# Optimization experiments

Measured on AMD Instinct MI355X. Metric: run time of the kernel, lower is better.

The kernel has to match this reference:

```python
import jax, jax.numpy as jnp
import numpy as np

N = 50000      # nodes
E = 800000     # edges (avg degree 16)
D = 64         # num_node_features
H = 64         # hidden_channels
G = 512        # graphs in batch
OUT = 32       # final linear output
NEG_SLOPE = 0.2


def setup_inputs() -> dict:
    key = jax.random.key(0)
    ks = jax.random.split(key, 20)
    s = 0.1  # param init scale
    inp = {
        "x": jax.random.normal(ks[0], (N, D), jnp.float32),
        "edge_index": jax.random.randint(ks[1], (2, E), 0, N, dtype=jnp.int64),
        "batch": jnp.sort(jax.random.randint(ks[2], (N,), 0, G, dtype=jnp.int64)),
        # GATv2 layer 1 (D -> H)
        "Wl1": jax.random.normal(ks[3], (D, H), jnp.float32) * s,
        "bl1": jnp.zeros((H,), jnp.float32),
        "Wr1": jax.random.normal(ks[4], (D, H), jnp.float32) * s,
        "br1": jnp.zeros((H,), jnp.float32),
        "att1": jax.random.normal(ks[5], (H,), jnp.float32) * s,
        "bias1": jnp.zeros((H,), jnp.float32),
        # GATv2 layer 2 (H -> H)
        "Wl2": jax.random.normal(ks[6], (H, H), jnp.float32) * s,
        "bl2": jnp.zeros((H,), jnp.float32),
        "Wr2": jax.random.normal(ks[7], (H, H), jnp.float32) * s,
        "br2": jnp.zeros((H,), jnp.float32),
        "att2": jax.random.normal(ks[8], (H,), jnp.float32) * s,
        "bias2": jnp.zeros((H,), jnp.float32),
        # final classifier
        "lin_w": jax.random.normal(ks[9], (H, OUT), jnp.float32) * s,
        "lin_b": jnp.zeros((OUT,), jnp.float32),
    }
    return inp


def _gatv2(x, src, dst, Wl, bl, Wr, br, att, bias):
    # GATv2Conv, heads=1, PyG semantics: messages flow src -> dst
    xl = x @ Wl + bl                       # [N, H] source transform (also the message)
    xr = x @ Wr + br                       # [N, H] destination transform
    z = xl[src] + xr[dst]                  # [E, H] gather
    e = jax.nn.leaky_relu(z, NEG_SLOPE) @ att  # [E] edge scores
    # segment softmax over edges grouped by destination node
    m = jax.ops.segment_max(e, dst, num_segments=N)   # [N]
    ex = jnp.exp(e - m[dst])                          # [E]
    denom = jax.ops.segment_sum(ex, dst, num_segments=N)  # [N]
    alpha = ex / denom[dst]                            # [E]
    out = jax.ops.segment_sum(alpha[:, None] * xl[src], dst, num_segments=N)  # [N, H]
    return out + bias


def reference(x, edge_index, batch,
              Wl1, bl1, Wr1, br1, att1, bias1,
              Wl2, bl2, Wr2, br2, att2, bias2,
              lin_w, lin_b):
    src, dst = edge_index[0], edge_index[1]
    h = jax.nn.relu(_gatv2(x, src, dst, Wl1, bl1, Wr1, br1, att1, bias1))
    h = jax.nn.relu(_gatv2(h, src, dst, Wl2, bl2, Wr2, br2, att2, bias2))
    # global mean pool over graphs
    sums = jax.ops.segment_sum(h, batch, num_segments=G)          # [G, H]
    cnts = jax.ops.segment_sum(jnp.ones((h.shape[0],), h.dtype), batch, num_segments=G)
    pooled = sums / jnp.maximum(cnts, 1.0)[:, None]
    # dropout(p=0.5) is identity at inference
    return pooled @ lin_w + lin_b                                  # [G, 32]
```

## Files before the change

kernel.cpp:

```cpp
#include <hip/hip_runtime.h>
#include <hip/hip_fp16.h>
#include <math.h>


#define ELLC    48
#define OVF_CAP 65536
#define ECHUNK  2048

typedef int      vint4 __attribute__((ext_vector_type(4)));
typedef _Float16 half4 __attribute__((ext_vector_type(4)));
typedef float    f32x4 __attribute__((ext_vector_type(4)));

#define GROWS 32
template <typename T>
__device__ __forceinline__ void dual_gemm_slim(
    int bid, int t,
    const T* __restrict__ X,
    const float* __restrict__ Wl, const float* __restrict__ bl,
    const float* __restrict__ Wr, const float* __restrict__ br,
    _Float16* __restrict__ xl, float* __restrict__ xr, int n,
    float* xS) {
    int row0 = bid * GROWS;
    for (int i = t; i < GROWS * 16; i += 256) {
        int r = row0 + (i >> 4);
        f32x4 v;
        v[0] = 0.f; v[1] = 0.f; v[2] = 0.f; v[3] = 0.f;
        if (r < n) {
            if constexpr (sizeof(T) == 2) {
                half4 hv = __builtin_nontemporal_load(
                    &((const half4*)(X + (size_t)r * 64))[i & 15]);
                v[0] = (float)hv[0]; v[1] = (float)hv[1];
                v[2] = (float)hv[2]; v[3] = (float)hv[3];
            } else {
                v = __builtin_nontemporal_load(
                    &((const f32x4*)(X + (size_t)r * 64))[i & 15]);
            }
        }
        ((f32x4*)xS)[i] = v;
    }
    __syncthreads();
    int h  = t & 63;
    int rb = t >> 6;
    float accl[8], accr[8];
#pragma unroll
    for (int i = 0; i < 8; ++i) { accl[i] = 0.f; accr[i] = 0.f; }
#pragma unroll 4
    for (int d = 0; d < 64; ++d) {
        float wl = Wl[d * 64 + h];
        float wr = Wr[d * 64 + h];
#pragma unroll
        for (int i = 0; i < 8; ++i) {
            float xv = xS[(rb + 4 * i) * 64 + d];
            accl[i] += xv * wl;
            accr[i] += xv * wr;
        }
    }
    float blv = bl[h], brv = br[h];
#pragma unroll
    for (int i = 0; i < 8; ++i) {
        int r = row0 + rb + 4 * i;
        if (r < n) {
            __builtin_nontemporal_store((_Float16)(accl[i] + blv),
                                        &xl[(size_t)r * 64 + h]);
            __builtin_nontemporal_store(accr[i] + brv,
                                        &xr[(size_t)r * 64 + h]);
        }
    }
}

__global__ __launch_bounds__(256) void dual_gemm64_f16_kernel(
    const _Float16* __restrict__ X,
    const float* __restrict__ Wl, const float* __restrict__ bl,
    const float* __restrict__ Wr, const float* __restrict__ br,
    _Float16* __restrict__ xl, float* __restrict__ xr, int n) {
    __shared__ float xS[GROWS * 64];
    dual_gemm_slim<_Float16>(blockIdx.x, threadIdx.x, X, Wl, bl, Wr, br,
                             xl, xr, n, xS);
}

__global__ __launch_bounds__(256) void fill_gemm_kernel(
    const int* __restrict__ src, const int* __restrict__ dst,
    int* __restrict__ cnt, unsigned short* __restrict__ ell,
    int* __restrict__ novf, int* __restrict__ ovf_dst, int* __restrict__ ovf_src,
    int E, int N, int psize, int fb, int ggrid,
    const float* __restrict__ X,
    const float* __restrict__ Wl, const float* __restrict__ bl,
    const float* __restrict__ Wr, const float* __restrict__ br,
    _Float16* __restrict__ xl, float* __restrict__ xr) {
    __shared__ float xS[GROWS * 64];
    int b = blockIdx.x;
    int q = b / 24, r = b % 24;
    if (r >= 16) {
        int vg = q * 8 + (r - 16);
        if (vg < ggrid)
            dual_gemm_slim<float>(vg, threadIdx.x, X, Wl, bl, Wr, br,
                                  xl, xr, N, xS);
        return;
    }
    int vb = q * 16 + r;
    if (vb >= fb) return;
    int t     = threadIdx.x;
    int chunk = vb >> 3;
    int p     = vb & 7;
    int d0    = p * psize;
    int d1    = min(N, d0 + psize);
    int e0    = chunk * ECHUNK;
    int e1    = min(E, e0 + ECHUNK);
    int nq    = (e1 - e0) >> 2;
    const vint4* dst4 = (const vint4*)(dst + e0);
    const vint4* src4 = (const vint4*)(src + e0);

    auto scatter4 = [&](vint4 dv, vint4 sv) {
#pragma unroll
        for (int k = 0; k < 4; ++k) {
            int d = dv[k];
            int s = sv[k];
            if (d >= d0 && d < d1) {
                int pos = atomicAdd(&cnt[d], 1);
                if (pos < ELLC) {
                    ell[d * ELLC + pos] = (unsigned short)s;
                } else {
                    int j = atomicAdd(novf, 1);
                    if (j < OVF_CAP) { ovf_dst[j] = d; ovf_src[j] = s; }
                }
            }
        }
    };

    if (nq == (ECHUNK >> 2)) {
        vint4 dvA = __builtin_nontemporal_load(&dst4[t]);
        vint4 svA = __builtin_nontemporal_load(&src4[t]);
        vint4 dvB = __builtin_nontemporal_load(&dst4[t + 256]);
        vint4 svB = __builtin_nontemporal_load(&src4[t + 256]);
        scatter4(dvA, svA);
        scatter4(dvB, svB);
    } else {
        for (int qq = t; qq < nq; qq += 256) {
            vint4 dv = __builtin_nontemporal_load(&dst4[qq]);
            vint4 sv = __builtin_nontemporal_load(&src4[qq]);
            scatter4(dv, sv);
        }
        for (int e = e0 + (nq << 2) + t; e < e1; e += 256) {
            int d = dst[e];
            if (d >= d0 && d < d1) {
                int pos = atomicAdd(&cnt[d], 1);
                int s   = src[e];
                if (pos < ELLC) {
                    ell[d * ELLC + pos] = (unsigned short)s;
                } else {
                    int j = atomicAdd(novf, 1);
                    if (j < OVF_CAP) { ovf_dst[j] = d; ovf_src[j] = s; }
                }
            }
        }
    }
}

__global__ __launch_bounds__(256) void gat_aggregate_kernel(
    const _Float16* __restrict__ xl, const float* __restrict__ xr,
    const int* __restrict__ cnt, const unsigned short* __restrict__ ell,
    const int* __restrict__ novf, const int* __restrict__ ovf_dst,
    const int* __restrict__ ovf_src,
    const float* __restrict__ att, const float* __restrict__ bias,
    _Float16* __restrict__ out, int n) {
    int wid  = (blockIdx.x * blockDim.x + threadIdx.x) >> 6;
    int lane = threadIdx.x & 63;
    if (wid >= n) return;
    int g = lane >> 4;
    int l = lane & 15;
    int d = wid;

    float4 att4 = ((const float4*)att)[l];
    float4 b4   = ((const float4*)bias)[l];
    int deg_d = cnt[d];
    int nd  = min(deg_d, ELLC);
    int beg = d * ELLC;

    float  s   = 0.f;
    float4 acc = make_float4(0.f, 0.f, 0.f, 0.f);

    if (deg_d > 0) {
        int myidx = 0;
        if (lane < ELLC)
            myidx = (int)__builtin_nontemporal_load(&ell[beg + lane]);
        int i_first = __shfl(myidx, 0);

        f32x4 xrt = __builtin_nontemporal_load(
            &((const f32x4*)(xr + (size_t)d * 64))[l]);
        float4 xr4 = make_float4(xrt[0], xrt[1], xrt[2], xrt[3]);

#pragma unroll 6
        for (int k = 0; k * 8 < nd; ++k) {
            int  sa = k * 8 + g, sb = sa + 4;
            bool aa = sa < nd,   ab = sb < nd;
            int  i0 = __shfl(myidx, sa); if (!aa) i0 = i_first;
            int  i1 = __shfl(myidx, sb); if (!ab) i1 = i_first;
            half4 h0 = ((const half4*)(xl + (size_t)i0 * 64))[l];
            half4 h1 = ((const half4*)(xl + (size_t)i1 * 64))[l];
            float4 x0 = make_float4((float)h0[0], (float)h0[1], (float)h0[2], (float)h0[3]);
            float4 x1 = make_float4((float)h1[0], (float)h1[1], (float)h1[2], (float)h1[3]);
            float z, c0 = 0.f, c1 = 0.f;
            z = x0.x + xr4.x; c0 += ((z > 0.f) ? z : 0.2f * z) * att4.x;
            z = x0.y + xr4.y; c0 += ((z > 0.f) ? z : 0.2f * z) * att4.y;
            z = x0.z + xr4.z; c0 += ((z > 0.f) ? z : 0.2f * z) * att4.z;
            z = x0.w + xr4.w; c0 += ((z > 0.f) ? z : 0.2f * z) * att4.w;
            z = x1.x + xr4.x; c1 += ((z > 0.f) ? z : 0.2f * z) * att4.x;
            z = x1.y + xr4.y; c1 += ((z > 0.f) ? z : 0.2f * z) * att4.y;
            z = x1.z + xr4.z; c1 += ((z > 0.f) ? z : 0.2f * z) * att4.z;
            z = x1.w + xr4.w; c1 += ((z > 0.f) ? z : 0.2f * z) * att4.w;
#pragma unroll
            for (int sh = 8; sh >= 1; sh >>= 1) {
                c0 += __shfl_xor(c0, sh);
                c1 += __shfl_xor(c1, sh);
            }
            float w0 = aa ? __expf(fminf(c0, 30.f)) : 0.f;
            float w1 = ab ? __expf(fminf(c1, 30.f)) : 0.f;
            s += w0 + w1;
            acc.x += w0 * x0.x + w1 * x1.x;
            acc.y += w0 * x0.y + w1 * x1.y;
            acc.z += w0 * x0.z + w1 * x1.z;
            acc.w += w0 * x0.w + w1 * x1.w;
        }
        if (deg_d > ELLC) {
            int no = min(*novf, OVF_CAP);
            for (int j = g; j < no; j += 4) {
                bool active = (ovf_dst[j] == d);
                int  i0     = active ? ovf_src[j] : i_first;
                half4 h0 = ((const half4*)(xl + (size_t)i0 * 64))[l];
                float4 x0 = make_float4((float)h0[0], (float)h0[1], (float)h0[2], (float)h0[3]);
                float z, c0 = 0.f;
                z = x0.x + xr4.x; c0 += ((z > 0.f) ? z : 0.2f * z) * att4.x;
                z = x0.y + xr4.y; c0 += ((z > 0.f) ? z : 0.2f * z) * att4.y;
                z = x0.z + xr4.z; c0 += ((z > 0.f) ? z : 0.2f * z) * att4.z;
                z = x0.w + xr4.w; c0 += ((z > 0.f) ? z : 0.2f * z) * att4.w;
#pragma unroll
                for (int sh = 8; sh >= 1; sh >>= 1) c0 += __shfl_xor(c0, sh);
                float w0 = active ? __expf(fminf(c0, 30.f)) : 0.f;
                s += w0;
                acc.x += w0 * x0.x;
                acc.y += w0 * x0.y;
                acc.z += w0 * x0.z;
                acc.w += w0 * x0.w;
            }
        }
#pragma unroll
        for (int mask = 16; mask <= 32; mask <<= 1) {
            s     += __shfl_xor(s, mask);
            acc.x += __shfl_xor(acc.x, mask);
            acc.y += __shfl_xor(acc.y, mask);
            acc.z += __shfl_xor(acc.z, mask);
            acc.w += __shfl_xor(acc.w, mask);
        }
    }
    if (g == 0) {
        float inv = (s > 0.f) ? (1.f / s) : 0.f;
        half4 hv;
        hv[0] = (_Float16)fmaxf(acc.x * inv + b4.x, 0.f);
        hv[1] = (_Float16)fmaxf(acc.y * inv + b4.y, 0.f);
        hv[2] = (_Float16)fmaxf(acc.z * inv + b4.z, 0.f);
        hv[3] = (_Float16)fmaxf(acc.w * inv + b4.w, 0.f);
        __builtin_nontemporal_store(hv, (half4*)(out + (size_t)d * 64) + l);
    }
}

__global__ __launch_bounds__(256) void pool_final_kernel(
    const _Float16* __restrict__ h, const int* __restrict__ batch,
    const float* __restrict__ lin_w, const float* __restrict__ lin_b,
    float* __restrict__ out, int N, int G) {
    int g = blockIdx.x;
    int t = threadIdx.x;
    auto lb = [&](int key) {
        int lo = 0, hi = N;
        while (lo < hi) {
            int mid = (lo + hi) >> 1;
            if (batch[mid] < key) lo = mid + 1; else hi = mid;
        }
        return lo;
    };
    int start = lb(g), end = lb(g + 1);

    __shared__ float part[4][64];
    __shared__ float pooled[64];
    int f = t & 63, w = t >> 6;
    float acc = 0.f;
    for (int i = start + w; i < end; i += 4)
        acc += (float)__builtin_nontemporal_load(&h[(size_t)i * 64 + f]);
    part[w][f] = acc;
    __syncthreads();
    if (t < 64) {
        float s = part[0][t] + part[1][t] + part[2][t] + part[3][t];
        pooled[t] = s / fmaxf((float)(end - start), 1.f);
    }
    __syncthreads();
    if (t < 32) {
        float a = 0.f;
#pragma unroll 8
        for (int hh = 0; hh < 64; ++hh) a += pooled[hh] * lin_w[hh * 32 + t];
        out[g * 32 + t] = a + lin_b[t];
    }
}

extern "C" void kernel_launch(void* const* d_in, const int* in_sizes, int n_in,
                              void* d_out, int out_size, void* d_ws, size_t ws_size,
                              hipStream_t stream) {
    const float* x     = (const float*)d_in[0];
    const int*   ei    = (const int*)d_in[1];
    const int*   batch = (const int*)d_in[2];
    const float* Wl1   = (const float*)d_in[3];
    const float* bl1   = (const float*)d_in[4];
    const float* Wr1   = (const float*)d_in[5];
    const float* br1   = (const float*)d_in[6];
    const float* att1  = (const float*)d_in[7];
    const float* bias1 = (const float*)d_in[8];
    const float* Wl2   = (const float*)d_in[9];
    const float* bl2   = (const float*)d_in[10];
    const float* Wr2   = (const float*)d_in[11];
    const float* br2   = (const float*)d_in[12];
    const float* att2  = (const float*)d_in[13];
    const float* bias2 = (const float*)d_in[14];
    const float* lin_w = (const float*)d_in[15];
    const float* lin_b = (const float*)d_in[16];
    float* out = (float*)d_out;

    const int N = in_sizes[0] / 64;
    const int E = in_sizes[1] / 2;
    const int G = out_size / 32;
    const int* src = ei;
    const int* dst = ei + E;

    char*  ws  = (char*)d_ws;
    size_t off = 0;
    auto alloc = [&](size_t bytes) -> void* {
        void* p = ws + off;
        off += bytes;
        off = (off + 255) & ~(size_t)255;
        return p;
    };
    _Float16* xl   = (_Float16*)alloc((size_t)N * 64 * sizeof(_Float16));
    float* xr      = (float*)alloc((size_t)N * 64 * sizeof(float));
    _Float16* h1   = (_Float16*)alloc((size_t)N * 64 * sizeof(_Float16));
    int*   cnt     = (int*)alloc((size_t)N * sizeof(int));
    int*   novf    = (int*)alloc(256);
    char*  zend    = ws + off;
    unsigned short* ell = (unsigned short*)alloc((size_t)N * ELLC * sizeof(unsigned short));
    int*   ovf_dst = (int*)alloc((size_t)OVF_CAP * sizeof(int));
    int*   ovf_src = (int*)alloc((size_t)OVF_CAP * sizeof(int));

    (void)hipMemsetAsync(cnt, 0, (size_t)(zend - (char*)cnt), stream);

    int ggrid  = (N + GROWS - 1) / GROWS;
    int agrid  = (N + 3) / 4;
    int nchunk = (E + ECHUNK - 1) / ECHUNK;
    int fb     = nchunk * 8;
    int psize  = (N + 7) / 8;
    int ngroups = max((fb + 15) / 16, (ggrid + 7) / 8);
    int igrid   = ngroups * 24;

    fill_gemm_kernel<<<igrid, 256, 0, stream>>>(
        src, dst, cnt, ell, novf, ovf_dst, ovf_src, E, N, psize, fb, ggrid,
        x, Wl1, bl1, Wr1, br1, xl, xr);

    gat_aggregate_kernel<<<agrid, 256, 0, stream>>>(
        xl, xr, cnt, ell, novf, ovf_dst, ovf_src, att1, bias1, h1, N);

    dual_gemm64_f16_kernel<<<ggrid, 256, 0, stream>>>(
        h1, Wl2, bl2, Wr2, br2, xl, xr, N);

    gat_aggregate_kernel<<<agrid, 256, 0, stream>>>(
        xl, xr, cnt, ell, novf, ovf_dst, ovf_src, att2, bias2, h1, N);

    pool_final_kernel<<<G, 256, 0, stream>>>(h1, batch, lin_w, lin_b, out, N, G);
}
```

Measured before the change: 249.6 us.

## Fuse layer-1 aggregation with layer-2 dual GEMM via shared-memory staging

Replaces the separate layer-1 aggregate kernel and the layer-2 dual GEMM kernel with one kernel. Each block aggregates 32 destination rows (8 per wavefront) into LDS in fp32, then runs the dual GEMM on them directly. This removes a launch and the fp16 h1 round trip through global memory, and drops the fp16 rounding of h1. In exchange each block processes rows serially per wave, which lowers parallelism for the gather-heavy phase, and separate xl2/xr2 buffers are allocated.

```diff
diff --git a/kernel.cpp b/kernel.cpp
--- a/kernel.cpp
+++ b/kernel.cpp
@@ -12,33 +12,26 @@
 typedef float    f32x4 __attribute__((ext_vector_type(4)));
 
 #define GROWS 32
-template <typename T>
-__device__ __forceinline__ void dual_gemm_slim(
-    int bid, int t,
-    const T* __restrict__ X,
-    const float* __restrict__ Wl, const float* __restrict__ bl,
-    const float* __restrict__ Wr, const float* __restrict__ br,
-    _Float16* __restrict__ xl, float* __restrict__ xr, int n,
-    float* xS) {
-    int row0 = bid * GROWS;
+
+__device__ __forceinline__ void stage_rows_f32(
+    int row0, int t, const float* __restrict__ X, int n, float* xS) {
     for (int i = t; i < GROWS * 16; i += 256) {
         int r = row0 + (i >> 4);
         f32x4 v;
         v[0] = 0.f; v[1] = 0.f; v[2] = 0.f; v[3] = 0.f;
-        if (r < n) {
-            if constexpr (sizeof(T) == 2) {
-                half4 hv = __builtin_nontemporal_load(
-                    &((const half4*)(X + (size_t)r * 64))[i & 15]);
-                v[0] = (float)hv[0]; v[1] = (float)hv[1];
-                v[2] = (float)hv[2]; v[3] = (float)hv[3];
-            } else {
-                v = __builtin_nontemporal_load(
-                    &((const f32x4*)(X + (size_t)r * 64))[i & 15]);
-            }
-        }
+        if (r < n)
+            v = __builtin_nontemporal_load(
+                &((const f32x4*)(X + (size_t)r * 64))[i & 15]);
         ((f32x4*)xS)[i] = v;
     }
-    __syncthreads();
+}
+
+__device__ __forceinline__ void gemm_compute(
+    int row0, int t,
+    const float* __restrict__ Wl, const float* __restrict__ bl,
+    const float* __restrict__ Wr, const float* __restrict__ br,
+    _Float16* __restrict__ xl, float* __restrict__ xr, int n,
+    const float* xS) {
     int h  = t & 63;
     int rb = t >> 6;
     float accl[8], accr[8];
@@ -66,16 +59,6 @@
                                         &xr[(size_t)r * 64 + h]);
         }
     }
-}
-
-__global__ __launch_bounds__(256) void dual_gemm64_f16_kernel(
-    const _Float16* __restrict__ X,
-    const float* __restrict__ Wl, const float* __restrict__ bl,
-    const float* __restrict__ Wr, const float* __restrict__ br,
-    _Float16* __restrict__ xl, float* __restrict__ xr, int n) {
-    __shared__ float xS[GROWS * 64];
-    dual_gemm_slim<_Float16>(blockIdx.x, threadIdx.x, X, Wl, bl, Wr, br,
-                             xl, xr, n, xS);
 }
 
 __global__ __launch_bounds__(256) void fill_gemm_kernel(
@@ -92,9 +75,11 @@
     int q = b / 24, r = b % 24;
     if (r >= 16) {
         int vg = q * 8 + (r - 16);
-        if (vg < ggrid)
-            dual_gemm_slim<float>(vg, threadIdx.x, X, Wl, bl, Wr, br,
-                                  xl, xr, N, xS);
+        if (vg < ggrid) {
+            stage_rows_f32(vg * GROWS, threadIdx.x, X, N, xS);
+            __syncthreads();
+            gemm_compute(vg * GROWS, threadIdx.x, Wl, bl, Wr, br, xl, xr, N, xS);
+        }
         return;
     }
     int vb = q * 16 + r;
@@ -156,6 +141,138 @@
     }
 }
 
+__device__ __forceinline__ void agg_row(
+    int d, int lane, int g, int l,
+    const _Float16* __restrict__ xl, const float* __restrict__ xr,
+    const int* __restrict__ cnt, const unsigned short* __restrict__ ell,
+    const int* __restrict__ novf, const int* __restrict__ ovf_dst,
+    const int* __restrict__ ovf_src,
+    float4 att4, float& s, float4& acc, int& deg_d) {
+    deg_d = cnt[d];
+    int nd  = min(deg_d, ELLC);
+    int beg = d * ELLC;
+    s = 0.f;
+    acc = make_float4(0.f, 0.f, 0.f, 0.f);
+    if (deg_d <= 0) return;
+
+    int myidx = 0;
+    if (lane < ELLC)
+        myidx = (int)__builtin_nontemporal_load(&ell[beg + lane]);
+    int i_first = __shfl(myidx, 0);
+
+    f32x4 xrt = __builtin_nontemporal_load(
+        &((const f32x4*)(xr + (size_t)d * 64))[l]);
+    float4 xr4 = make_float4(xrt[0], xrt[1], xrt[2], xrt[3]);
+
+#pragma unroll 6
+    for (int k = 0; k * 8 < nd; ++k) {
+        int  sa = k * 8 + g, sb = sa + 4;
+        bool aa = sa < nd,   ab = sb < nd;
+        int  i0 = __shfl(myidx, sa); if (!aa) i0 = i_first;
+        int  i1 = __shfl(myidx, sb); if (!ab) i1 = i_first;
+        half4 h0 = ((const half4*)(xl + (size_t)i0 * 64))[l];
+        half4 h1 = ((const half4*)(xl + (size_t)i1 * 64))[l];
+        float4 x0 = make_float4((float)h0[0], (float)h0[1], (float)h0[2], (float)h0[3]);
+        float4 x1 = make_float4((float)h1[0], (float)h1[1], (float)h1[2], (float)h1[3]);
+        float z, c0 = 0.f, c1 = 0.f;
+        z = x0.x + xr4.x; c0 += ((z > 0.f) ? z : 0.2f * z) * att4.x;
+        z = x0.y + xr4.y; c0 += ((z > 0.f) ? z : 0.2f * z) * att4.y;
+        z = x0.z + xr4.z; c0 += ((z > 0.f) ? z : 0.2f * z) * att4.z;
+        z = x0.w + xr4.w; c0 += ((z > 0.f) ? z : 0.2f * z) * att4.w;
+        z = x1.x + xr4.x; c1 += ((z > 0.f) ? z : 0.2f * z) * att4.x;
+        z = x1.y + xr4.y; c1 += ((z > 0.f) ? z : 0.2f * z) * att4.y;
+        z = x1.z + xr4.z; c1 += ((z > 0.f) ? z : 0.2f * z) * att4.z;
+        z = x1.w + xr4.w; c1 += ((z > 0.f) ? z : 0.2f * z) * att4.w;
+#pragma unroll
+        for (int sh = 8; sh >= 1; sh >>= 1) {
+            c0 += __shfl_xor(c0, sh);
+            c1 += __shfl_xor(c1, sh);
+        }
+        float w0 = aa ? __expf(fminf(c0, 30.f)) : 0.f;
+        float w1 = ab ? __expf(fminf(c1, 30.f)) : 0.f;
+        s += w0 + w1;
+        acc.x += w0 * x0.x + w1 * x1.x;
+        acc.y += w0 * x0.y + w1 * x1.y;
+        acc.z += w0 * x0.z + w1 * x1.z;
+        acc.w += w0 * x0.w + w1 * x1.w;
+    }
+    if (deg_d > ELLC) {
+        int no = min(*novf, OVF_CAP);
+        for (int j = g; j < no; j += 4) {
+            bool active = (ovf_dst[j] == d);
+            int  i0     = active ? ovf_src[j] : i_first;
+            half4 h0 = ((const half4*)(xl + (size_t)i0 * 64))[l];
+            float4 x0 = make_float4((float)h0[0], (float)h0[1], (float)h0[2], (float)h0[3]);
+            f32x4 xrt2 = ((const f32x4*)(xr + (size_t)d * 64))[l];
+            float z, c0 = 0.f;
+            z = x0.x + xrt2[0]; c0 += ((z > 0.f) ? z : 0.2f * z) * att4.x;
+            z = x0.y + xrt2[1]; c0 += ((z > 0.f) ? z : 0.2f * z) * att4.y;
+            z = x0.z + xrt2[2]; c0 += ((z > 0.f) ? z : 0.2f * z) * att4.z;
+            z = x0.w + xrt2[3]; c0 += ((z > 0.f) ? z : 0.2f * z) * att4.w;
+#pragma unroll
+            for (int sh = 8; sh >= 1; sh >>= 1) c0 += __shfl_xor(c0, sh);
+            float w0 = active ? __expf(fminf(c0, 30.f)) : 0.f;
+            s += w0;
+            acc.x += w0 * x0.x;
+            acc.y += w0 * x0.y;
+            acc.z += w0 * x0.z;
+            acc.w += w0 * x0.w;
+        }
+    }
+#pragma unroll
+    for (int mask = 16; mask <= 32; mask <<= 1) {
+        s     += __shfl_xor(s, mask);
+        acc.x += __shfl_xor(acc.x, mask);
+        acc.y += __shfl_xor(acc.y, mask);
+        acc.z += __shfl_xor(acc.z, mask);
+        acc.w += __shfl_xor(acc.w, mask);
+    }
+}
+
+__global__ __launch_bounds__(256) void agg_gemm_kernel(
+    const _Float16* __restrict__ xl1, const float* __restrict__ xr1,
+    const int* __restrict__ cnt, const unsigned short* __restrict__ ell,
+    const int* __restrict__ novf, const int* __restrict__ ovf_dst,
+    const int* __restrict__ ovf_src,
+    const float* __restrict__ att, const float* __restrict__ bias,
+    const float* __restrict__ Wl2, const float* __restrict__ bl2,
+    const float* __restrict__ Wr2, const float* __restrict__ br2,
+    _Float16* __restrict__ xl2, float* __restrict__ xr2, int n) {
+    __shared__ float xS[GROWS * 64];
+    int t    = threadIdx.x;
+    int w    = t >> 6;
+    int lane = t & 63;
+    int g    = lane >> 4;
+    int l    = lane & 15;
+    int row0 = blockIdx.x * GROWS;
+
+    float4 att4 = ((const float4*)att)[l];
+    float4 b4   = ((const float4*)bias)[l];
+
+    for (int i = 0; i < 8; ++i) {
+        int rr = w * 8 + i;
+        int d  = row0 + rr;
+        float s; float4 acc; int deg_d;
+        if (d < n) {
+            agg_row(d, lane, g, l, xl1, xr1, cnt, ell, novf, ovf_dst, ovf_src,
+                    att4, s, acc, deg_d);
+        } else { s = 0.f; acc = make_float4(0.f, 0.f, 0.f, 0.f); }
+        if (g == 0) {
+            float4 hv = make_float4(0.f, 0.f, 0.f, 0.f);
+            if (d < n) {
+                float inv = (s > 0.f) ? (1.f / s) : 0.f;
+                hv.x = fmaxf(acc.x * inv + b4.x, 0.f);
+                hv.y = fmaxf(acc.y * inv + b4.y, 0.f);
+                hv.z = fmaxf(acc.z * inv + b4.z, 0.f);
+                hv.w = fmaxf(acc.w * inv + b4.w, 0.f);
+            }
+            ((float4*)(xS + rr * 64))[l] = hv;
+        }
+    }
+    __syncthreads();
+    gemm_compute(row0, t, Wl2, bl2, Wr2, br2, xl2, xr2, n, xS);
+}
+
 __global__ __launch_bounds__(256) void gat_aggregate_kernel(
     const _Float16* __restrict__ xl, const float* __restrict__ xr,
     const int* __restrict__ cnt, const unsigned short* __restrict__ ell,
@@ -168,90 +285,11 @@
     if (wid >= n) return;
     int g = lane >> 4;
     int l = lane & 15;
-    int d = wid;
-
     float4 att4 = ((const float4*)att)[l];
     float4 b4   = ((const float4*)bias)[l];
-    int deg_d = cnt[d];
-    int nd  = min(deg_d, ELLC);
-    int beg = d * ELLC;
-
-    float  s   = 0.f;
-    float4 acc = make_float4(0.f, 0.f, 0.f, 0.f);
-
-    if (deg_d > 0) {
-        int myidx = 0;
-        if (lane < ELLC)
-            myidx = (int)__builtin_nontemporal_load(&ell[beg + lane]);
-        int i_first = __shfl(myidx, 0);
-
-        f32x4 xrt = __builtin_nontemporal_load(
-            &((const f32x4*)(xr + (size_t)d * 64))[l]);
-        float4 xr4 = make_float4(xrt[0], xrt[1], xrt[2], xrt[3]);
-
-#pragma unroll 6
-        for (int k = 0; k * 8 < nd; ++k) {
-            int  sa = k * 8 + g, sb = sa + 4;
-            bool aa = sa < nd,   ab = sb < nd;
-            int  i0 = __shfl(myidx, sa); if (!aa) i0 = i_first;
-            int  i1 = __shfl(myidx, sb); if (!ab) i1 = i_first;
-            half4 h0 = ((const half4*)(xl + (size_t)i0 * 64))[l];
-            half4 h1 = ((const half4*)(xl + (size_t)i1 * 64))[l];
-            float4 x0 = make_float4((float)h0[0], (float)h0[1], (float)h0[2], (float)h0[3]);
-            float4 x1 = make_float4((float)h1[0], (float)h1[1], (float)h1[2], (float)h1[3]);
-            float z, c0 = 0.f, c1 = 0.f;
-            z = x0.x + xr4.x; c0 += ((z > 0.f) ? z : 0.2f * z) * att4.x;
-            z = x0.y + xr4.y; c0 += ((z > 0.f) ? z : 0.2f * z) * att4.y;
-            z = x0.z + xr4.z; c0 += ((z > 0.f) ? z : 0.2f * z) * att4.z;
-            z = x0.w + xr4.w; c0 += ((z > 0.f) ? z : 0.2f * z) * att4.w;
-            z = x1.x + xr4.x; c1 += ((z > 0.f) ? z : 0.2f * z) * att4.x;
-            z = x1.y + xr4.y; c1 += ((z > 0.f) ? z : 0.2f * z) * att4.y;
-            z = x1.z + xr4.z; c1 += ((z > 0.f) ? z : 0.2f * z) * att4.z;
-            z = x1.w + xr4.w; c1 += ((z > 0.f) ? z : 0.2f * z) * att4.w;
-#pragma unroll
-            for (int sh = 8; sh >= 1; sh >>= 1) {
-                c0 += __shfl_xor(c0, sh);
-                c1 += __shfl_xor(c1, sh);
-            }
-            float w0 = aa ? __expf(fminf(c0, 30.f)) : 0.f;
-            float w1 = ab ? __expf(fminf(c1, 30.f)) : 0.f;
-            s += w0 + w1;
-            acc.x += w0 * x0.x + w1 * x1.x;
-            acc.y += w0 * x0.y + w1 * x1.y;
-            acc.z += w0 * x0.z + w1 * x1.z;
-            acc.w += w0 * x0.w + w1 * x1.w;
-        }
-        if (deg_d > ELLC) {
-            int no = min(*novf, OVF_CAP);
-            for (int j = g; j < no; j += 4) {
-                bool active = (ovf_dst[j] == d);
-                int  i0     = active ? ovf_src[j] : i_first;
-                half4 h0 = ((const half4*)(xl + (size_t)i0 * 64))[l];
-                float4 x0 = make_float4((float)h0[0], (float)h0[1], (float)h0[2], (float)h0[3]);
-                float z, c0 = 0.f;
-                z = x0.x + xr4.x; c0 += ((z > 0.f) ? z : 0.2f * z) * att4.x;
-                z = x0.y + xr4.y; c0 += ((z > 0.f) ? z : 0.2f * z) * att4.y;
-                z = x0.z + xr4.z; c0 += ((z > 0.f) ? z : 0.2f * z) * att4.z;
-                z = x0.w + xr4.w; c0 += ((z > 0.f) ? z : 0.2f * z) * att4.w;
-#pragma unroll
-                for (int sh = 8; sh >= 1; sh >>= 1) c0 += __shfl_xor(c0, sh);
-                float w0 = active ? __expf(fminf(c0, 30.f)) : 0.f;
-                s += w0;
-                acc.x += w0 * x0.x;
-                acc.y += w0 * x0.y;
-                acc.z += w0 * x0.z;
-                acc.w += w0 * x0.w;
-            }
-        }
-#pragma unroll
-        for (int mask = 16; mask <= 32; mask <<= 1) {
-            s     += __shfl_xor(s, mask);
-            acc.x += __shfl_xor(acc.x, mask);
-            acc.y += __shfl_xor(acc.y, mask);
-            acc.z += __shfl_xor(acc.z, mask);
-            acc.w += __shfl_xor(acc.w, mask);
-        }
-    }
+    float s; float4 acc; int deg_d;
+    agg_row(wid, lane, g, l, xl, xr, cnt, ell, novf, ovf_dst, ovf_src,
+            att4, s, acc, deg_d);
     if (g == 0) {
         float inv = (s > 0.f) ? (1.f / s) : 0.f;
         half4 hv;
@@ -259,7 +297,7 @@
         hv[1] = (_Float16)fmaxf(acc.y * inv + b4.y, 0.f);
         hv[2] = (_Float16)fmaxf(acc.z * inv + b4.z, 0.f);
         hv[3] = (_Float16)fmaxf(acc.w * inv + b4.w, 0.f);
-        __builtin_nontemporal_store(hv, (half4*)(out + (size_t)d * 64) + l);
+        __builtin_nontemporal_store(hv, (half4*)(out + (size_t)wid * 64) + l);
     }
 }
 
@@ -336,9 +374,11 @@
         off = (off + 255) & ~(size_t)255;
         return p;
     };
-    _Float16* xl   = (_Float16*)alloc((size_t)N * 64 * sizeof(_Float16));
-    float* xr      = (float*)alloc((size_t)N * 64 * sizeof(float));
-    _Float16* h1   = (_Float16*)alloc((size_t)N * 64 * sizeof(_Float16));
+    _Float16* xl1  = (_Float16*)alloc((size_t)N * 64 * sizeof(_Float16));
+    float* xr1     = (float*)alloc((size_t)N * 64 * sizeof(float));
+    _Float16* xl2  = (_Float16*)alloc((size_t)N * 64 * sizeof(_Float16));
+    float* xr2     = (float*)alloc((size_t)N * 64 * sizeof(float));
+    _Float16* h2   = (_Float16*)alloc((size_t)N * 64 * sizeof(_Float16));
     int*   cnt     = (int*)alloc((size_t)N * sizeof(int));
     int*   novf    = (int*)alloc(256);
     char*  zend    = ws + off;
@@ -358,16 +398,14 @@
 
     fill_gemm_kernel<<<igrid, 256, 0, stream>>>(
         src, dst, cnt, ell, novf, ovf_dst, ovf_src, E, N, psize, fb, ggrid,
-        x, Wl1, bl1, Wr1, br1, xl, xr);
+        x, Wl1, bl1, Wr1, br1, xl1, xr1);
+
+    agg_gemm_kernel<<<ggrid, 256, 0, stream>>>(
+        xl1, xr1, cnt, ell, novf, ovf_dst, ovf_src, att1, bias1,
+        Wl2, bl2, Wr2, br2, xl2, xr2, N);
 
     gat_aggregate_kernel<<<agrid, 256, 0, stream>>>(
-        xl, xr, cnt, ell, novf, ovf_dst, ovf_src, att1, bias1, h1, N);
-
-    dual_gemm64_f16_kernel<<<ggrid, 256, 0, stream>>>(
-        h1, Wl2, bl2, Wr2, br2, xl, xr, N);
-
-    gat_aggregate_kernel<<<agrid, 256, 0, stream>>>(
-        xl, xr, cnt, ell, novf, ovf_dst, ovf_src, att2, bias2, h1, N);
-
-    pool_final_kernel<<<G, 256, 0, stream>>>(h1, batch, lin_w, lin_b, out, N, G);
-}
+        xl2, xr2, cnt, ell, novf, ovf_dst, ovf_src, att2, bias2, h2, N);
+
+    pool_final_kernel<<<G, 256, 0, stream>>>(h2, batch, lin_w, lin_b, out, N, G);
+}
```

Measured after the change: 247.9 us. About the same (-0.7%).
